# Performance work log

Hardware: AMD Instinct MI355X
Metric: run time of the kernel (lower is better)

## Reference

```python
import jax, jax.numpy as jnp
import numpy as np

B, T, D, NPER, E = 32, 256, 1024, 64, 65536
N = B * NPER  # total nodes
LN_EPS = 1e-5


def setup_inputs() -> dict:
    key = jax.random.key(0)
    ks = jax.random.split(key, 12)
    sc = 0.02  # init scale for weights
    inp = {
        "x": jax.random.normal(ks[0], (B, T, D), jnp.float32),
        "batch": jnp.repeat(jnp.arange(B, dtype=jnp.int32), NPER),
        "edge_index": jax.random.randint(ks[1], (2, E), 0, N, dtype=jnp.int32),
        "edge_distance_vec": jax.random.normal(ks[2], (E, 3), jnp.float32),
        "edge_distance": jax.random.uniform(ks[3], (E,), jnp.float32) + 0.5,
        "natoms": NPER,
        # energy head params: LayerNorm -> Linear(D,D) -> GELU -> Linear(D,1)
        "ln_g": jnp.ones((D,), jnp.float32),
        "ln_b": jnp.zeros((D,), jnp.float32),
        "We1": jax.random.normal(ks[4], (D, D), jnp.float32) * sc,
        "be1": jnp.zeros((D,), jnp.float32),
        "We2": jax.random.normal(ks[5], (D, 1), jnp.float32) * sc,
        "be2": jnp.zeros((1,), jnp.float32),
        # forces head params: Linear(2D,D) -> GELU -> Linear(D,1)
        "Wf1": jax.random.normal(ks[6], (2 * D, D), jnp.float32) * sc,
        "bf1": jnp.zeros((D,), jnp.float32),
        "Wf2": jax.random.normal(ks[7], (D, 1), jnp.float32) * sc,
        "bf2": jnp.zeros((1,), jnp.float32),
    }
    return inp


def reference(x, batch, edge_index, edge_distance_vec, edge_distance, natoms,
              ln_g, ln_b, We1, be1, We2, be2, Wf1, bf1, Wf2, bf2):
    # ---- energy head on CLS token ----
    cls = x[:, 0]  # [B, D]
    mu = jnp.mean(cls, axis=-1, keepdims=True)
    var = jnp.mean(jnp.square(cls - mu), axis=-1, keepdims=True)
    h = (cls - mu) / jnp.sqrt(var + LN_EPS) * ln_g + ln_b
    h = jax.nn.gelu(h @ We1 + be1, approximate=False)
    energy = h @ We2 + be2  # [B, 1]

    # ---- forces head: gather node pairs -> MLP -> scale -> scatter-sum ----
    # padded_node_mask selects tokens 1..natoms per graph; boolean indexing
    # flattens row-major, identical to this slice+reshape.
    nodes = x[:, 1:1 + natoms].reshape(-1, x.shape[-1])  # [N, D]
    ei0, ei1 = edge_index[0], edge_index[1]
    edge_inputs = jnp.concatenate([nodes[ei0], nodes[ei1]], axis=1)  # [E, 2D]
    fm = jax.nn.gelu(edge_inputs @ Wf1 + bf1, approximate=False) @ Wf2 + bf2  # [E, 1]
    force_pairs = fm * edge_distance_vec / edge_distance[:, None]  # [E, 3]
    forces = jax.ops.segment_sum(force_pairs, ei0, num_segments=batch.shape[0])  # [N, 3]
    return energy, forces
```

## Files before the change

### kernel.cpp

```cpp
#include <hip/hip_runtime.h>
#include <math.h>

#define BB 32
#define TT 256
#define DD 1024
#define NNODES 2048
#define EE 65536
#define LN_EPS 1e-5f

typedef __attribute__((ext_vector_type(8))) short shortx8;
typedef __attribute__((ext_vector_type(4))) float floatx4;
typedef __attribute__((ext_vector_type(8))) unsigned short ushortx8;

__device__ __forceinline__ float gelu_fast(float x) {
    float x2 = x * x;
    float z = x * fmaf(0.10294456f, x2, 2.30211786f);
    float e = __builtin_amdgcn_exp2f(z);
    float r = __builtin_amdgcn_rcpf(1.0f + e);
    return fmaf(-x, r, x);
}

__device__ __forceinline__ unsigned short f32_to_bf16(float f) {
    unsigned u = __float_as_uint(f);
    unsigned r = (u + 0x7FFF + ((u >> 16) & 1)) >> 16;
    return (unsigned short)r;
}

__device__ __forceinline__ float bf16_to_f32(unsigned short h) {
    return __uint_as_float(((unsigned)h) << 16);
}

__device__ __forceinline__ void load_lds16(const void* g, void* l) {
    __builtin_amdgcn_global_load_lds(
        (const __attribute__((address_space(1))) void*)g,
        (__attribute__((address_space(3))) void*)l, 16, 0, 0);
}

__global__ void zero_ln_kernel(const float* __restrict__ x,
                               const float* __restrict__ g,
                               const float* __restrict__ bta,
                               float* __restrict__ hnorm,
                               float* __restrict__ out) {
    __shared__ float red[256];
    int b = blockIdx.x;
    int t = threadIdx.x;
    int zi = b * 256 + t;
    if (zi < BB + NNODES * 3) out[zi] = 0.0f;
    const float* row = x + (size_t)b * TT * DD;
    float v[4];
    float s = 0.0f;
    #pragma unroll
    for (int j = 0; j < 4; ++j) { v[j] = row[t + j * 256]; s += v[j]; }
    red[t] = s; __syncthreads();
    for (int off = 128; off > 0; off >>= 1) {
        if (t < off) red[t] += red[t + off];
        __syncthreads();
    }
    float mu = red[0] * (1.0f / DD);
    __syncthreads();
    float sq = 0.0f;
    #pragma unroll
    for (int j = 0; j < 4; ++j) { float d = v[j] - mu; sq += d * d; }
    red[t] = sq; __syncthreads();
    for (int off = 128; off > 0; off >>= 1) {
        if (t < off) red[t] += red[t + off];
        __syncthreads();
    }
    float rstd = rsqrtf(red[0] * (1.0f / DD) + LN_EPS);
    #pragma unroll
    for (int j = 0; j < 4; ++j) {
        int d = t + j * 256;
        hnorm[b * DD + d] = (v[j] - mu) * rstd * g[d] + bta[d];
    }
}

__global__ __launch_bounds__(256) void energy1_kernel(
    const float* __restrict__ hnorm, const float* __restrict__ We1,
    float* __restrict__ He) {
    __shared__ float hs[64 * 16];
    int t = threadIdx.x;
    int col = blockIdx.x * 256 + t;
    int k0 = blockIdx.y * 64;
    int r0 = blockIdx.z * 16;
    for (int idx = t; idx < 64 * 16; idx += 256) {
        int r = idx & 15, k = idx >> 4;
        hs[idx] = hnorm[(size_t)(r0 + r) * DD + k0 + k];
    }
    __syncthreads();
    float acc[16];
    #pragma unroll
    for (int r = 0; r < 16; ++r) acc[r] = 0.0f;
    #pragma unroll 4
    for (int k = 0; k < 64; ++k) {
        float w = We1[(size_t)(k0 + k) * DD + col];
        const float* hrow = hs + k * 16;
        #pragma unroll
        for (int j = 0; j < 4; ++j) {
            float4 h4 = *(const float4*)(hrow + j * 4);
            acc[j * 4 + 0] = fmaf(h4.x, w, acc[j * 4 + 0]);
            acc[j * 4 + 1] = fmaf(h4.y, w, acc[j * 4 + 1]);
            acc[j * 4 + 2] = fmaf(h4.z, w, acc[j * 4 + 2]);
            acc[j * 4 + 3] = fmaf(h4.w, w, acc[j * 4 + 3]);
        }
    }
    float* o = He + (size_t)blockIdx.y * 32 * DD;
    #pragma unroll
    for (int r = 0; r < 16; ++r) o[(size_t)(r0 + r) * DD + col] = acc[r];
}

__global__ __launch_bounds__(256) void energy2_kernel(
    const float* __restrict__ He, const float* __restrict__ be1,
    const float* __restrict__ We2, const float* __restrict__ be2,
    float* __restrict__ out) {
    __shared__ float red[256];
    int b = blockIdx.x;
    int t = threadIdx.x;
    float p = 0.0f;
    #pragma unroll
    for (int j = 0; j < 4; ++j) {
        int c = t * 4 + j;
        float s = 0.0f;
        #pragma unroll
        for (int ks = 0; ks < 16; ++ks) s += He[(size_t)ks * 32 * DD + b * DD + c];
        s += be1[c];
        p += gelu_fast(s) * We2[c];
    }
    red[t] = p; __syncthreads();
    for (int off = 128; off > 0; off >>= 1) {
        if (t < off) red[t] += red[t + off];
        __syncthreads();
    }
    if (t == 0) out[b] = red[0] + be2[0];
}

__global__ __launch_bounds__(256) void prep_kernel(
    const float* __restrict__ x, const float* __restrict__ Wf1,
    unsigned short* __restrict__ nodesB, unsigned short* __restrict__ Wf1T) {
    __shared__ float tile[32][33];
    if (blockIdx.x < 2048) {
        int idx4 = (blockIdx.x * 256 + threadIdx.x) * 4;
        int i = idx4 >> 10;
        int k = idx4 & 1023;
        const float* src = x + ((size_t)(i >> 6) * TT + 1 + (i & 63)) * DD + k;
        float4 v = *(const float4*)src;
        ushort4 o;
        o.x = f32_to_bf16(v.x); o.y = f32_to_bf16(v.y);
        o.z = f32_to_bf16(v.z); o.w = f32_to_bf16(v.w);
        *(ushort4*)&nodesB[idx4] = o;
    } else {
        int q = blockIdx.x - 2048;
        int tx = threadIdx.x & 31;
        int ty = threadIdx.x >> 5;
        int n0 = (q & 31) * 32;
        int kg0 = (q >> 5) * 32;
        #pragma unroll
        for (int j = 0; j < 4; ++j) {
            int r = ty * 4 + j;
            tile[r][tx] = Wf1[(size_t)(kg0 + r) * DD + n0 + tx];
        }
        __syncthreads();
        int half = kg0 >> 10;
        int kk0 = kg0 & 1023;
        unsigned short* o = Wf1T + (size_t)half * DD * DD;
        #pragma unroll
        for (int j = 0; j < 4; ++j) {
            int rn = ty * 4 + j;
            o[(size_t)(n0 + rn) * DD + kk0 + tx] = f32_to_bf16(tile[tx][rn]);
        }
    }
}

__global__ __launch_bounds__(256) void pgemm_mfma_kernel(
    const unsigned short* __restrict__ nodesB,
    const unsigned short* __restrict__ Wf1T, const float* __restrict__ bf1,
    unsigned short* __restrict__ P) {
    __shared__ unsigned short As[128 * 64];
    __shared__ unsigned short Bs[128 * 64];
    int t = threadIdx.x;
    int w = t >> 6;
    int lane = t & 63;
    int quad = lane >> 4;
    int l16 = lane & 15;
    int wn = (w & 1) * 64;
    int wi = (w >> 1) * 64;
    int half = blockIdx.z;
    int n0 = blockIdx.x * 128;
    int i0 = blockIdx.y * 128;

    const unsigned short* Ag = Wf1T + (size_t)half * DD * DD;
    const unsigned short* Bg = nodesB;

    int sr = lane >> 3;
    int sc = (lane & 7) ^ sr;
    size_t aoff[4], boff[4];
    #pragma unroll
    for (int j = 0; j < 4; ++j) {
        aoff[j] = (size_t)(n0 + w * 32 + j * 8 + sr) * DD + sc * 8;
        boff[j] = (size_t)(i0 + w * 32 + j * 8 + sr) * DD + sc * 8;
    }

    floatx4 acc[4][4];
    #pragma unroll
    for (int a = 0; a < 4; ++a)
        #pragma unroll
        for (int b = 0; b < 4; ++b) {
            acc[a][b][0] = 0.f; acc[a][b][1] = 0.f;
            acc[a][b][2] = 0.f; acc[a][b][3] = 0.f;
        }

    for (int k0 = 0; k0 < DD; k0 += 64) {
        #pragma unroll
        for (int j = 0; j < 4; ++j) {
            load_lds16(Ag + aoff[j] + k0, (void*)(As + (w * 32 + j * 8) * 64));
            load_lds16(Bg + boff[j] + k0, (void*)(Bs + (w * 32 + j * 8) * 64));
        }
        __syncthreads();
        #pragma unroll
        for (int s = 0; s < 2; ++s) {
            shortx8 af[4], bfr[4];
            #pragma unroll
            for (int f = 0; f < 4; ++f) {
                int rn = wn + f * 16 + l16;
                af[f] = *(const shortx8*)&As[rn * 64 + ((((s << 2) | quad) ^ (rn & 7)) << 3)];
                int ri = wi + f * 16 + l16;
                bfr[f] = *(const shortx8*)&Bs[ri * 64 + ((((s << 2) | quad) ^ (ri & 7)) << 3)];
            }
            #pragma unroll
            for (int fa = 0; fa < 4; ++fa)
                #pragma unroll
                for (int fb = 0; fb < 4; ++fb)
                    acc[fa][fb] = __builtin_amdgcn_mfma_f32_16x16x32_bf16(
                        af[fa], bfr[fb], acc[fa][fb], 0, 0, 0);
        }
        __syncthreads();
    }

    unsigned short* Pout = P + (size_t)half * NNODES * DD;
    #pragma unroll
    for (int fa = 0; fa < 4; ++fa) {
        int n = n0 + wn + fa * 16 + quad * 4;
        float4 badd = make_float4(0.f, 0.f, 0.f, 0.f);
        if (half == 0) badd = *(const float4*)(bf1 + n);
        #pragma unroll
        for (int fb = 0; fb < 4; ++fb) {
            int i = i0 + wi + fb * 16 + l16;
            floatx4 v = acc[fa][fb];
            ushort4 o;
            o.x = f32_to_bf16(v[0] + badd.x);
            o.y = f32_to_bf16(v[1] + badd.y);
            o.z = f32_to_bf16(v[2] + badd.z);
            o.w = f32_to_bf16(v[3] + badd.w);
            *(ushort4*)&Pout[(size_t)i * DD + n] = o;
        }
    }
}

__global__ __launch_bounds__(256) void edge_kernel(
    const unsigned short* __restrict__ P, const int* __restrict__ edge_index,
    const float* __restrict__ evec, const float* __restrict__ edist,
    const float* __restrict__ Wf2, const float* __restrict__ bf2,
    float* __restrict__ forces) {
    int lane = threadIdx.x & 63;
    int wv = blockIdx.x * 4 + (threadIdx.x >> 6);
    int dbase = lane * 8;
    float wreg[16];
    #pragma unroll
    for (int s = 0; s < 2; ++s) {
        float4 a = *(const float4*)(Wf2 + s * 512 + dbase);
        float4 b = *(const float4*)(Wf2 + s * 512 + dbase + 4);
        wreg[s * 8 + 0] = a.x; wreg[s * 8 + 1] = a.y;
        wreg[s * 8 + 2] = a.z; wreg[s * 8 + 3] = a.w;
        wreg[s * 8 + 4] = b.x; wreg[s * 8 + 5] = b.y;
        wreg[s * 8 + 6] = b.z; wreg[s * 8 + 7] = b.w;
    }
    float bias2 = bf2[0];
    const unsigned short* P1 = P + (size_t)NNODES * DD;
    #pragma unroll
    for (int it = 0; it < 4; ++it) {
        int ea = wv + (2 * it) * 8192;
        int eb = wv + (2 * it + 1) * 8192;
        int i0a = edge_index[ea], i1a = edge_index[EE + ea];
        int i0b = edge_index[eb], i1b = edge_index[EE + eb];
        const unsigned short* p0a = P + (size_t)i0a * DD + dbase;
        const unsigned short* p1a = P1 + (size_t)i1a * DD + dbase;
        const unsigned short* p0b = P + (size_t)i0b * DD + dbase;
        const unsigned short* p1b = P1 + (size_t)i1b * DD + dbase;
        ushortx8 u0a[2], u1a[2], u0b[2], u1b[2];
        #pragma unroll
        for (int s = 0; s < 2; ++s) {
            u0a[s] = *(const ushortx8*)(p0a + s * 512);
            u1a[s] = *(const ushortx8*)(p1a + s * 512);
            u0b[s] = *(const ushortx8*)(p0b + s * 512);
            u1b[s] = *(const ushortx8*)(p1b + s * 512);
        }
        float acca = 0.0f, accb = 0.0f;
        #pragma unroll
        for (int s = 0; s < 2; ++s) {
            #pragma unroll
            for (int j = 0; j < 8; ++j) {
                float ha = bf16_to_f32((unsigned short)u0a[s][j]) +
                           bf16_to_f32((unsigned short)u1a[s][j]);
                float hb = bf16_to_f32((unsigned short)u0b[s][j]) +
                           bf16_to_f32((unsigned short)u1b[s][j]);
                acca = fmaf(gelu_fast(ha), wreg[s * 8 + j], acca);
                accb = fmaf(gelu_fast(hb), wreg[s * 8 + j], accb);
            }
        }
        acca += __shfl_xor(acca, 32, 64);
        accb += __shfl_xor(accb, 32, 64);
        float red = (lane < 32) ? acca : accb;
        #pragma unroll
        for (int off = 16; off > 0; off >>= 1) red += __shfl_xor(red, off, 64);
        float fm = red + bias2;
        int l5 = lane & 31;
        if (l5 < 3) {
            int e = (lane < 32) ? ea : eb;
            int i0 = (lane < 32) ? i0a : i0b;
            float sc = fm / edist[e];
            atomicAdd(&forces[i0 * 3 + l5], sc * evec[e * 3 + l5]);
        }
    }
}

extern "C" void kernel_launch(void* const* d_in, const int* in_sizes, int n_in,
                              void* d_out, int out_size, void* d_ws, size_t ws_size,
                              hipStream_t stream) {
    const float* x    = (const float*)d_in[0];
    const int* edge_index = (const int*)d_in[2];
    const float* evec = (const float*)d_in[3];
    const float* edist = (const float*)d_in[4];
    const float* ln_g = (const float*)d_in[6];
    const float* ln_b = (const float*)d_in[7];
    const float* We1  = (const float*)d_in[8];
    const float* be1  = (const float*)d_in[9];
    const float* We2  = (const float*)d_in[10];
    const float* be2  = (const float*)d_in[11];
    const float* Wf1  = (const float*)d_in[12];
    const float* bf1  = (const float*)d_in[13];
    const float* Wf2  = (const float*)d_in[14];
    const float* bf2  = (const float*)d_in[15];

    float* out = (float*)d_out;

    char* wsb = (char*)d_ws;
    unsigned short* P      = (unsigned short*)(wsb);
    float* hnorm           = (float*)(wsb);
    float* He              = (float*)(wsb + (128 << 10));
    unsigned short* nodesB = (unsigned short*)(wsb + (8u << 20));
    unsigned short* Wf1T   = (unsigned short*)(wsb + (12u << 20));

    zero_ln_kernel<<<BB, 256, 0, stream>>>(x, ln_g, ln_b, hnorm, out);
    energy1_kernel<<<dim3(4, 16, 2), 256, 0, stream>>>(hnorm, We1, He);
    energy2_kernel<<<BB, 256, 0, stream>>>(He, be1, We2, be2, out);
    prep_kernel<<<4096, 256, 0, stream>>>(x, Wf1, nodesB, Wf1T);
    pgemm_mfma_kernel<<<dim3(8, 16, 2), 256, 0, stream>>>(nodesB, Wf1T, bf1, P);
    edge_kernel<<<2048, 256, 0, stream>>>(P, edge_index, evec, edist, Wf2, bf2,
                                          out + BB);
}
```

Baseline: 178.0 us.

## Merge six launches into three by co-scheduling energy head with forces stages

Folds the LayerNorm/zero, energy GEMM and energy reduction kernels into the prep, MFMA GEMM and edge kernels as extra block ranges, so three launches replace six. The MFMA GEMM is reshaped to 512-thread blocks with a per-wave 32x64 sub-tile and a flattened 1D grid. Workspace offsets are moved so hnorm/He no longer alias P. The aim is less launch overhead and filling idle CUs with the small energy work, at the cost of fewer accumulators per wave in the GEMM.

```diff
diff --git a/kernel.cpp b/kernel.cpp
--- a/kernel.cpp
+++ b/kernel.cpp
@@ -36,109 +36,49 @@
         (__attribute__((address_space(3))) void*)l, 16, 0, 0);
 }
 
-__global__ void zero_ln_kernel(const float* __restrict__ x,
-                               const float* __restrict__ g,
-                               const float* __restrict__ bta,
-                               float* __restrict__ hnorm,
-                               float* __restrict__ out) {
-    __shared__ float red[256];
+__global__ __launch_bounds__(256) void k1_zero_ln_prep_kernel(
+    const float* __restrict__ x, const float* __restrict__ g,
+    const float* __restrict__ bta, const float* __restrict__ Wf1,
+    float* __restrict__ hnorm, float* __restrict__ out,
+    unsigned short* __restrict__ nodesB, unsigned short* __restrict__ Wf1T) {
+    __shared__ float smem[32 * 33];
+    int t = threadIdx.x;
     int b = blockIdx.x;
-    int t = threadIdx.x;
-    int zi = b * 256 + t;
-    if (zi < BB + NNODES * 3) out[zi] = 0.0f;
-    const float* row = x + (size_t)b * TT * DD;
-    float v[4];
-    float s = 0.0f;
-    #pragma unroll
-    for (int j = 0; j < 4; ++j) { v[j] = row[t + j * 256]; s += v[j]; }
-    red[t] = s; __syncthreads();
-    for (int off = 128; off > 0; off >>= 1) {
-        if (t < off) red[t] += red[t + off];
+    if (b < BB) {
+        int zi = b * 256 + t;
+        if (zi < BB + NNODES * 3) out[zi] = 0.0f;
+        float* red = smem;
+        const float* row = x + (size_t)b * TT * DD;
+        float v[4];
+        float s = 0.0f;
+        #pragma unroll
+        for (int j = 0; j < 4; ++j) { v[j] = row[t + j * 256]; s += v[j]; }
+        red[t] = s; __syncthreads();
+        for (int off = 128; off > 0; off >>= 1) {
+            if (t < off) red[t] += red[t + off];
+            __syncthreads();
+        }
+        float mu = red[0] * (1.0f / DD);
         __syncthreads();
-    }
-    float mu = red[0] * (1.0f / DD);
-    __syncthreads();
-    float sq = 0.0f;
-    #pragma unroll
-    for (int j = 0; j < 4; ++j) { float d = v[j] - mu; sq += d * d; }
-    red[t] = sq; __syncthreads();
-    for (int off = 128; off > 0; off >>= 1) {
-        if (t < off) red[t] += red[t + off];
-        __syncthreads();
-    }
-    float rstd = rsqrtf(red[0] * (1.0f / DD) + LN_EPS);
-    #pragma unroll
-    for (int j = 0; j < 4; ++j) {
-        int d = t + j * 256;
-        hnorm[b * DD + d] = (v[j] - mu) * rstd * g[d] + bta[d];
-    }
-}
-
-__global__ __launch_bounds__(256) void energy1_kernel(
-    const float* __restrict__ hnorm, const float* __restrict__ We1,
-    float* __restrict__ He) {
-    __shared__ float hs[64 * 16];
-    int t = threadIdx.x;
-    int col = blockIdx.x * 256 + t;
-    int k0 = blockIdx.y * 64;
-    int r0 = blockIdx.z * 16;
-    for (int idx = t; idx < 64 * 16; idx += 256) {
-        int r = idx & 15, k = idx >> 4;
-        hs[idx] = hnorm[(size_t)(r0 + r) * DD + k0 + k];
-    }
-    __syncthreads();
-    float acc[16];
-    #pragma unroll
-    for (int r = 0; r < 16; ++r) acc[r] = 0.0f;
-    #pragma unroll 4
-    for (int k = 0; k < 64; ++k) {
-        float w = We1[(size_t)(k0 + k) * DD + col];
-        const float* hrow = hs + k * 16;
+        float sq = 0.0f;
+        #pragma unroll
+        for (int j = 0; j < 4; ++j) { float d = v[j] - mu; sq += d * d; }
+        red[t] = sq; __syncthreads();
+        for (int off = 128; off > 0; off >>= 1) {
+            if (t < off) red[t] += red[t + off];
+            __syncthreads();
+        }
+        float rstd = rsqrtf(red[0] * (1.0f / DD) + LN_EPS);
         #pragma unroll
         for (int j = 0; j < 4; ++j) {
-            float4 h4 = *(const float4*)(hrow + j * 4);
-            acc[j * 4 + 0] = fmaf(h4.x, w, acc[j * 4 + 0]);
-            acc[j * 4 + 1] = fmaf(h4.y, w, acc[j * 4 + 1]);
-            acc[j * 4 + 2] = fmaf(h4.z, w, acc[j * 4 + 2]);
-            acc[j * 4 + 3] = fmaf(h4.w, w, acc[j * 4 + 3]);
-        }
-    }
-    float* o = He + (size_t)blockIdx.y * 32 * DD;
-    #pragma unroll
-    for (int r = 0; r < 16; ++r) o[(size_t)(r0 + r) * DD + col] = acc[r];
-}
-
-__global__ __launch_bounds__(256) void energy2_kernel(
-    const float* __restrict__ He, const float* __restrict__ be1,
-    const float* __restrict__ We2, const float* __restrict__ be2,
-    float* __restrict__ out) {
-    __shared__ float red[256];
-    int b = blockIdx.x;
-    int t = threadIdx.x;
-    float p = 0.0f;
-    #pragma unroll
-    for (int j = 0; j < 4; ++j) {
-        int c = t * 4 + j;
-        float s = 0.0f;
-        #pragma unroll
-        for (int ks = 0; ks < 16; ++ks) s += He[(size_t)ks * 32 * DD + b * DD + c];
-        s += be1[c];
-        p += gelu_fast(s) * We2[c];
-    }
-    red[t] = p; __syncthreads();
-    for (int off = 128; off > 0; off >>= 1) {
-        if (t < off) red[t] += red[t + off];
-        __syncthreads();
-    }
-    if (t == 0) out[b] = red[0] + be2[0];
-}
-
-__global__ __launch_bounds__(256) void prep_kernel(
-    const float* __restrict__ x, const float* __restrict__ Wf1,
-    unsigned short* __restrict__ nodesB, unsigned short* __restrict__ Wf1T) {
-    __shared__ float tile[32][33];
-    if (blockIdx.x < 2048) {
-        int idx4 = (blockIdx.x * 256 + threadIdx.x) * 4;
+            int d = t + j * 256;
+            hnorm[b * DD + d] = (v[j] - mu) * rstd * g[d] + bta[d];
+        }
+        return;
+    }
+    int pb = b - BB;
+    if (pb < 2048) {
+        int idx4 = (pb * 256 + t) * 4;
         int i = idx4 >> 10;
         int k = idx4 & 1023;
         const float* src = x + ((size_t)(i >> 6) * TT + 1 + (i & 63)) * DD + k;
@@ -148,9 +88,10 @@
         o.z = f32_to_bf16(v.z); o.w = f32_to_bf16(v.w);
         *(ushort4*)&nodesB[idx4] = o;
     } else {
-        int q = blockIdx.x - 2048;
-        int tx = threadIdx.x & 31;
-        int ty = threadIdx.x >> 5;
+        int q = pb - 2048;
+        float (*tile)[33] = (float(*)[33])smem;
+        int tx = t & 31;
+        int ty = t >> 5;
         int n0 = (q & 31) * 32;
         int kg0 = (q >> 5) * 32;
         #pragma unroll
@@ -170,155 +111,226 @@
     }
 }
 
-__global__ __launch_bounds__(256) void pgemm_mfma_kernel(
+__global__ __launch_bounds__(512) void k2_gemm_kernel(
     const unsigned short* __restrict__ nodesB,
     const unsigned short* __restrict__ Wf1T, const float* __restrict__ bf1,
-    unsigned short* __restrict__ P) {
-    __shared__ unsigned short As[128 * 64];
-    __shared__ unsigned short Bs[128 * 64];
+    unsigned short* __restrict__ P, const float* __restrict__ hnorm,
+    const float* __restrict__ We1, float* __restrict__ He) {
+    __shared__ unsigned short smem[2 * 128 * 64];
     int t = threadIdx.x;
-    int w = t >> 6;
-    int lane = t & 63;
-    int quad = lane >> 4;
-    int l16 = lane & 15;
-    int wn = (w & 1) * 64;
-    int wi = (w >> 1) * 64;
-    int half = blockIdx.z;
-    int n0 = blockIdx.x * 128;
-    int i0 = blockIdx.y * 128;
-
-    const unsigned short* Ag = Wf1T + (size_t)half * DD * DD;
-    const unsigned short* Bg = nodesB;
-
-    int sr = lane >> 3;
-    int sc = (lane & 7) ^ sr;
-    size_t aoff[4], boff[4];
-    #pragma unroll
-    for (int j = 0; j < 4; ++j) {
-        aoff[j] = (size_t)(n0 + w * 32 + j * 8 + sr) * DD + sc * 8;
-        boff[j] = (size_t)(i0 + w * 32 + j * 8 + sr) * DD + sc * 8;
-    }
-
-    floatx4 acc[4][4];
-    #pragma unroll
-    for (int a = 0; a < 4; ++a)
-        #pragma unroll
-        for (int b = 0; b < 4; ++b) {
-            acc[a][b][0] = 0.f; acc[a][b][1] = 0.f;
-            acc[a][b][2] = 0.f; acc[a][b][3] = 0.f;
-        }
-
-    for (int k0 = 0; k0 < DD; k0 += 64) {
-        #pragma unroll
-        for (int j = 0; j < 4; ++j) {
-            load_lds16(Ag + aoff[j] + k0, (void*)(As + (w * 32 + j * 8) * 64));
-            load_lds16(Bg + boff[j] + k0, (void*)(Bs + (w * 32 + j * 8) * 64));
+    int b = blockIdx.x;
+    if (b < 256) {
+        unsigned short* As = smem;
+        unsigned short* Bs = smem + 128 * 64;
+        int w = t >> 6;
+        int lane = t & 63;
+        int quad = lane >> 4;
+        int l16 = lane & 15;
+        int wn = (w & 3) * 32;
+        int wi = (w >> 2) * 64;
+        int n0 = (b & 7) * 128;
+        int i0 = ((b >> 3) & 15) * 128;
+        int half = b >> 7;
+
+        const unsigned short* Ag = Wf1T + (size_t)half * DD * DD;
+        const unsigned short* Bg = nodesB;
+
+        int sr = lane >> 3;
+        int sc = (lane & 7) ^ sr;
+        size_t aoff[2], boff[2];
+        #pragma unroll
+        for (int j = 0; j < 2; ++j) {
+            int row = w * 16 + j * 8;
+            aoff[j] = (size_t)(n0 + row + sr) * DD + sc * 8;
+            boff[j] = (size_t)(i0 + row + sr) * DD + sc * 8;
+        }
+
+        floatx4 acc[2][4];
+        #pragma unroll
+        for (int a = 0; a < 2; ++a)
+            #pragma unroll
+            for (int c = 0; c < 4; ++c) {
+                acc[a][c][0] = 0.f; acc[a][c][1] = 0.f;
+                acc[a][c][2] = 0.f; acc[a][c][3] = 0.f;
+            }
+
+        for (int k0 = 0; k0 < DD; k0 += 64) {
+            #pragma unroll
+            for (int j = 0; j < 2; ++j) {
+                int row = w * 16 + j * 8;
+                load_lds16(Ag + aoff[j] + k0, (void*)(As + row * 64));
+                load_lds16(Bg + boff[j] + k0, (void*)(Bs + row * 64));
+            }
+            __syncthreads();
+            #pragma unroll
+            for (int s = 0; s < 2; ++s) {
+                shortx8 af[2], bfr[4];
+                #pragma unroll
+                for (int f = 0; f < 2; ++f) {
+                    int rn = wn + f * 16 + l16;
+                    af[f] = *(const shortx8*)&As[rn * 64 + ((((s << 2) | quad) ^ (rn & 7)) << 3)];
+                }
+                #pragma unroll
+                for (int f = 0; f < 4; ++f) {
+                    int ri = wi + f * 16 + l16;
+                    bfr[f] = *(const shortx8*)&Bs[ri * 64 + ((((s << 2) | quad) ^ (ri & 7)) << 3)];
+                }
+                #pragma unroll
+                for (int fa = 0; fa < 2; ++fa)
+                    #pragma unroll
+                    for (int fb = 0; fb < 4; ++fb)
+                        acc[fa][fb] = __builtin_amdgcn_mfma_f32_16x16x32_bf16(
+                            af[fa], bfr[fb], acc[fa][fb], 0, 0, 0);
+            }
+            __syncthreads();
+        }
+
+        unsigned short* Pout = P + (size_t)half * NNODES * DD;
+        #pragma unroll
+        for (int fa = 0; fa < 2; ++fa) {
+            int n = n0 + wn + fa * 16 + quad * 4;
+            float4 badd = make_float4(0.f, 0.f, 0.f, 0.f);
+            if (half == 0) badd = *(const float4*)(bf1 + n);
+            #pragma unroll
+            for (int fb = 0; fb < 4; ++fb) {
+                int i = i0 + wi + fb * 16 + l16;
+                floatx4 v = acc[fa][fb];
+                ushort4 o;
+                o.x = f32_to_bf16(v[0] + badd.x);
+                o.y = f32_to_bf16(v[1] + badd.y);
+                o.z = f32_to_bf16(v[2] + badd.z);
+                o.w = f32_to_bf16(v[3] + badd.w);
+                *(ushort4*)&Pout[(size_t)i * DD + n] = o;
+            }
+        }
+        return;
+    }
+    {
+        int q = b - 256;
+        float* hs = (float*)smem;
+        int col = (q & 1) * 512 + t;
+        int k0 = ((q >> 1) & 15) * 64;
+        int r0 = (q >> 5) * 16;
+        for (int idx = t; idx < 64 * 16; idx += 512) {
+            int r = idx & 15, k = idx >> 4;
+            hs[idx] = hnorm[(size_t)(r0 + r) * DD + k0 + k];
         }
         __syncthreads();
-        #pragma unroll
-        for (int s = 0; s < 2; ++s) {
-            shortx8 af[4], bfr[4];
-            #pragma unroll
-            for (int f = 0; f < 4; ++f) {
-                int rn = wn + f * 16 + l16;
-                af[f] = *(const shortx8*)&As[rn * 64 + ((((s << 2) | quad) ^ (rn & 7)) << 3)];
-                int ri = wi + f * 16 + l16;
-                bfr[f] = *(const shortx8*)&Bs[ri * 64 + ((((s << 2) | quad) ^ (ri & 7)) << 3)];
-            }
-            #pragma unroll
-            for (int fa = 0; fa < 4; ++fa)
-                #pragma unroll
-                for (int fb = 0; fb < 4; ++fb)
-                    acc[fa][fb] = __builtin_amdgcn_mfma_f32_16x16x32_bf16(
-                        af[fa], bfr[fb], acc[fa][fb], 0, 0, 0);
-        }
-        __syncthreads();
-    }
-
-    unsigned short* Pout = P + (size_t)half * NNODES * DD;
-    #pragma unroll
-    for (int fa = 0; fa < 4; ++fa) {
-        int n = n0 + wn + fa * 16 + quad * 4;
-        float4 badd = make_float4(0.f, 0.f, 0.f, 0.f);
-        if (half == 0) badd = *(const float4*)(bf1 + n);
-        #pragma unroll
-        for (int fb = 0; fb < 4; ++fb) {
-            int i = i0 + wi + fb * 16 + l16;
-            floatx4 v = acc[fa][fb];
-            ushort4 o;
-            o.x = f32_to_bf16(v[0] + badd.x);
-            o.y = f32_to_bf16(v[1] + badd.y);
-            o.z = f32_to_bf16(v[2] + badd.z);
-            o.w = f32_to_bf16(v[3] + badd.w);
-            *(ushort4*)&Pout[(size_t)i * DD + n] = o;
-        }
-    }
-}
-
-__global__ __launch_bounds__(256) void edge_kernel(
+        float acc[16];
+        #pragma unroll
+        for (int r = 0; r < 16; ++r) acc[r] = 0.0f;
+        #pragma unroll 4
+        for (int k = 0; k < 64; ++k) {
+            float wv = We1[(size_t)(k0 + k) * DD + col];
+            const float* hrow = hs + k * 16;
+            #pragma unroll
+            for (int j = 0; j < 4; ++j) {
+                float4 h4 = *(const float4*)(hrow + j * 4);
+                acc[j * 4 + 0] = fmaf(h4.x, wv, acc[j * 4 + 0]);
+                acc[j * 4 + 1] = fmaf(h4.y, wv, acc[j * 4 + 1]);
+                acc[j * 4 + 2] = fmaf(h4.z, wv, acc[j * 4 + 2]);
+                acc[j * 4 + 3] = fmaf(h4.w, wv, acc[j * 4 + 3]);
+            }
+        }
+        float* o = He + (size_t)((q >> 1) & 15) * 32 * DD;
+        #pragma unroll
+        for (int r = 0; r < 16; ++r) o[(size_t)(r0 + r) * DD + col] = acc[r];
+    }
+}
+
+__global__ __launch_bounds__(256) void k3_edge_energy2_kernel(
     const unsigned short* __restrict__ P, const int* __restrict__ edge_index,
     const float* __restrict__ evec, const float* __restrict__ edist,
     const float* __restrict__ Wf2, const float* __restrict__ bf2,
-    float* __restrict__ forces) {
-    int lane = threadIdx.x & 63;
-    int wv = blockIdx.x * 4 + (threadIdx.x >> 6);
-    int dbase = lane * 8;
-    float wreg[16];
-    #pragma unroll
-    for (int s = 0; s < 2; ++s) {
-        float4 a = *(const float4*)(Wf2 + s * 512 + dbase);
-        float4 b = *(const float4*)(Wf2 + s * 512 + dbase + 4);
-        wreg[s * 8 + 0] = a.x; wreg[s * 8 + 1] = a.y;
-        wreg[s * 8 + 2] = a.z; wreg[s * 8 + 3] = a.w;
-        wreg[s * 8 + 4] = b.x; wreg[s * 8 + 5] = b.y;
-        wreg[s * 8 + 6] = b.z; wreg[s * 8 + 7] = b.w;
-    }
-    float bias2 = bf2[0];
-    const unsigned short* P1 = P + (size_t)NNODES * DD;
-    #pragma unroll
-    for (int it = 0; it < 4; ++it) {
-        int ea = wv + (2 * it) * 8192;
-        int eb = wv + (2 * it + 1) * 8192;
-        int i0a = edge_index[ea], i1a = edge_index[EE + ea];
-        int i0b = edge_index[eb], i1b = edge_index[EE + eb];
-        const unsigned short* p0a = P + (size_t)i0a * DD + dbase;
-        const unsigned short* p1a = P1 + (size_t)i1a * DD + dbase;
-        const unsigned short* p0b = P + (size_t)i0b * DD + dbase;
-        const unsigned short* p1b = P1 + (size_t)i1b * DD + dbase;
-        ushortx8 u0a[2], u1a[2], u0b[2], u1b[2];
+    const float* __restrict__ He, const float* __restrict__ be1,
+    const float* __restrict__ We2, const float* __restrict__ be2,
+    float* __restrict__ out) {
+    __shared__ float red[256];
+    int t = threadIdx.x;
+    int b = blockIdx.x;
+    if (b < 2048) {
+        float* forces = out + BB;
+        int lane = t & 63;
+        int wv = b * 4 + (t >> 6);
+        int dbase = lane * 8;
+        float wreg[16];
         #pragma unroll
         for (int s = 0; s < 2; ++s) {
-            u0a[s] = *(const ushortx8*)(p0a + s * 512);
-            u1a[s] = *(const ushortx8*)(p1a + s * 512);
-            u0b[s] = *(const ushortx8*)(p0b + s * 512);
-            u1b[s] = *(const ushortx8*)(p1b + s * 512);
-        }
-        float acca = 0.0f, accb = 0.0f;
-        #pragma unroll
-        for (int s = 0; s < 2; ++s) {
-            #pragma unroll
-            for (int j = 0; j < 8; ++j) {
-                float ha = bf16_to_f32((unsigned short)u0a[s][j]) +
-                           bf16_to_f32((unsigned short)u1a[s][j]);
-                float hb = bf16_to_f32((unsigned short)u0b[s][j]) +
-                           bf16_to_f32((unsigned short)u1b[s][j]);
-                acca = fmaf(gelu_fast(ha), wreg[s * 8 + j], acca);
-                accb = fmaf(gelu_fast(hb), wreg[s * 8 + j], accb);
-            }
-        }
-        acca += __shfl_xor(acca, 32, 64);
-        accb += __shfl_xor(accb, 32, 64);
-        float red = (lane < 32) ? acca : accb;
-        #pragma unroll
-        for (int off = 16; off > 0; off >>= 1) red += __shfl_xor(red, off, 64);
-        float fm = red + bias2;
-        int l5 = lane & 31;
-        if (l5 < 3) {
-            int e = (lane < 32) ? ea : eb;
-            int i0 = (lane < 32) ? i0a : i0b;
-            float sc = fm / edist[e];
-            atomicAdd(&forces[i0 * 3 + l5], sc * evec[e * 3 + l5]);
-        }
+            float4 a = *(const float4*)(Wf2 + s * 512 + dbase);
+            float4 c = *(const float4*)(Wf2 + s * 512 + dbase + 4);
+            wreg[s * 8 + 0] = a.x; wreg[s * 8 + 1] = a.y;
+            wreg[s * 8 + 2] = a.z; wreg[s * 8 + 3] = a.w;
+            wreg[s * 8 + 4] = c.x; wreg[s * 8 + 5] = c.y;
+            wreg[s * 8 + 6] = c.z; wreg[s * 8 + 7] = c.w;
+        }
+        float bias2 = bf2[0];
+        const unsigned short* P1 = P + (size_t)NNODES * DD;
+        #pragma unroll
+        for (int it = 0; it < 4; ++it) {
+            int ea = wv + (2 * it) * 8192;
+            int eb = wv + (2 * it + 1) * 8192;
+            int i0a = edge_index[ea], i1a = edge_index[EE + ea];
+            int i0b = edge_index[eb], i1b = edge_index[EE + eb];
+            const unsigned short* p0a = P + (size_t)i0a * DD + dbase;
+            const unsigned short* p1a = P1 + (size_t)i1a * DD + dbase;
+            const unsigned short* p0b = P + (size_t)i0b * DD + dbase;
+            const unsigned short* p1b = P1 + (size_t)i1b * DD + dbase;
+            ushortx8 u0a[2], u1a[2], u0b[2], u1b[2];
+            #pragma unroll
+            for (int s = 0; s < 2; ++s) {
+                u0a[s] = *(const ushortx8*)(p0a + s * 512);
+                u1a[s] = *(const ushortx8*)(p1a + s * 512);
+                u0b[s] = *(const ushortx8*)(p0b + s * 512);
+                u1b[s] = *(const ushortx8*)(p1b + s * 512);
+            }
+            float acca = 0.0f, accb = 0.0f;
+            #pragma unroll
+            for (int s = 0; s < 2; ++s) {
+                #pragma unroll
+                for (int j = 0; j < 8; ++j) {
+                    float ha = bf16_to_f32((unsigned short)u0a[s][j]) +
+                               bf16_to_f32((unsigned short)u1a[s][j]);
+                    float hb = bf16_to_f32((unsigned short)u0b[s][j]) +
+                               bf16_to_f32((unsigned short)u1b[s][j]);
+                    acca = fmaf(gelu_fast(ha), wreg[s * 8 + j], acca);
+                    accb = fmaf(gelu_fast(hb), wreg[s * 8 + j], accb);
+                }
+            }
+            acca += __shfl_xor(acca, 32, 64);
+            accb += __shfl_xor(accb, 32, 64);
+            float r = (lane < 32) ? acca : accb;
+            #pragma unroll
+            for (int off = 16; off > 0; off >>= 1) r += __shfl_xor(r, off, 64);
+            float fm = r + bias2;
+            int l5 = lane & 31;
+            if (l5 < 3) {
+                int e = (lane < 32) ? ea : eb;
+                int i0 = (lane < 32) ? i0a : i0b;
+                float sc = fm / edist[e];
+                atomicAdd(&forces[i0 * 3 + l5], sc * evec[e * 3 + l5]);
+            }
+        }
+        return;
+    }
+    {
+        int bb = b - 2048;
+        float p = 0.0f;
+        #pragma unroll
+        for (int j = 0; j < 4; ++j) {
+            int c = t * 4 + j;
+            float s = 0.0f;
+            #pragma unroll
+            for (int ks = 0; ks < 16; ++ks)
+                s += He[(size_t)ks * 32 * DD + bb * DD + c];
+            s += be1[c];
+            p += gelu_fast(s) * We2[c];
+        }
+        red[t] = p; __syncthreads();
+        for (int off = 128; off > 0; off >>= 1) {
+            if (t < off) red[t] += red[t + off];
+            __syncthreads();
+        }
+        if (t == 0) out[bb] = red[0] + be2[0];
     }
 }
 
@@ -344,16 +356,15 @@
 
     char* wsb = (char*)d_ws;
     unsigned short* P      = (unsigned short*)(wsb);
-    float* hnorm           = (float*)(wsb);
-    float* He              = (float*)(wsb + (128 << 10));
-    unsigned short* nodesB = (unsigned short*)(wsb + (8u << 20));
-    unsigned short* Wf1T   = (unsigned short*)(wsb + (12u << 20));
-
-    zero_ln_kernel<<<BB, 256, 0, stream>>>(x, ln_g, ln_b, hnorm, out);
-    energy1_kernel<<<dim3(4, 16, 2), 256, 0, stream>>>(hnorm, We1, He);
-    energy2_kernel<<<BB, 256, 0, stream>>>(He, be1, We2, be2, out);
-    prep_kernel<<<4096, 256, 0, stream>>>(x, Wf1, nodesB, Wf1T);
-    pgemm_mfma_kernel<<<dim3(8, 16, 2), 256, 0, stream>>>(nodesB, Wf1T, bf1, P);
-    edge_kernel<<<2048, 256, 0, stream>>>(P, edge_index, evec, edist, Wf2, bf2,
-                                          out + BB);
-}
+    float* hnorm           = (float*)(wsb + (8u << 20));
+    float* He              = (float*)(wsb + (8u << 20) + (128u << 10));
+    unsigned short* nodesB = (unsigned short*)(wsb + (11u << 20));
+    unsigned short* Wf1T   = (unsigned short*)(wsb + (16u << 20));
+
+    k1_zero_ln_prep_kernel<<<4128, 256, 0, stream>>>(x, ln_g, ln_b, Wf1, hnorm,
+                                                     out, nodesB, Wf1T);
+    k2_gemm_kernel<<<320, 512, 0, stream>>>(nodesB, Wf1T, bf1, P, hnorm, We1, He);
+    k3_edge_energy2_kernel<<<2080, 256, 0, stream>>>(P, edge_index, evec, edist,
+                                                     Wf2, bf2, He, be1, We2, be2,
+                                                     out);
+}
```

After: 158.0 us. 1.13x faster.
